# Kernel optimization log

Measured on AMD Instinct MI355X. Metric: run time of the kernel, lower is better.

## Reference

```python
import jax, jax.numpy as jnp
import numpy as np

LN_EPS = 1e-5

def _conv1d_same(x, w, b):
    # x: [B, L, Cin], w: [K, Cin, Cout] (kernel=3, padding=1 -> SAME)
    y = jax.lax.conv_general_dilated(x, w, window_strides=(1,), padding=[(1, 1)],
                                     dimension_numbers=('NWC', 'WIO', 'NWC'))
    return y + b

def _layer_norm(x, g, b):
    mu = jnp.mean(x, axis=-1, keepdims=True)
    var = jnp.var(x, axis=-1, keepdims=True)
    return (x - mu) * jax.lax.rsqrt(var + LN_EPS) * g + b

def _duration_predictor(x, conv1_w, conv1_b, ln1_g, ln1_b, conv2_w, conv2_b, ln2_g, ln2_b, lin_w, lin_b):
    h = jax.nn.relu(_layer_norm(_conv1d_same(x, conv1_w, conv1_b), ln1_g, ln1_b))
    h = jax.nn.relu(_layer_norm(_conv1d_same(h, conv2_w, conv2_b), ln2_g, ln2_b))
    out = jax.nn.relu(h @ lin_w + lin_b)  # [B, L, 1]
    return out[..., 0]  # squeeze -> [B, L]

def _length_regulate(x, dur, T):
    # Equivalent of alignment @ x without materializing [B, T, L] one-hot matrix.
    # Frame t copies phoneme j where cumsum(dur)[j-1] <= t < cumsum(dur)[j].
    ends = jnp.cumsum(dur, axis=-1)          # [B, L]
    total = ends[:, -1]                       # [B]
    t = jnp.arange(T)
    idx = jax.vmap(lambda e: jnp.searchsorted(e, t, side='right'))(ends)  # [B, T]
    idx = jnp.minimum(idx, dur.shape[1] - 1)
    gathered = jnp.take_along_axis(x, idx[:, :, None], axis=1)            # [B, T, D]
    mask = t[None, :] < total[:, None]                                    # [B, T]
    return jnp.where(mask[:, :, None], gathered, 0.0)

def setup_inputs() -> dict:
    key = jax.random.key(0)
    ks = jax.random.split(key, 8)
    B, L, D, F = 64, 512, 256, 256
    inp = {
        'x': jax.random.normal(ks[0], (B, L, D), dtype=jnp.float32),
        'target': jax.random.randint(ks[1], (B, L), 0, 8, dtype=jnp.int32),
        'mel_max_length': 4096,
        'conv1_w': jax.random.normal(ks[2], (3, D, F), dtype=jnp.float32) * 0.05,
        'conv1_b': jnp.zeros((F,), jnp.float32),
        'ln1_g': jnp.ones((F,), jnp.float32),
        'ln1_b': jnp.zeros((F,), jnp.float32),
        'conv2_w': jax.random.normal(ks[3], (3, F, F), dtype=jnp.float32) * 0.05,
        'conv2_b': jnp.zeros((F,), jnp.float32),
        'ln2_g': jnp.ones((F,), jnp.float32),
        'ln2_b': jnp.zeros((F,), jnp.float32),
        'lin_w': jax.random.normal(ks[4], (F, 1), dtype=jnp.float32) * 0.05,
        'lin_b': jnp.zeros((1,), jnp.float32),
    }
    return inp

def reference(x, target, mel_max_length, conv1_w, conv1_b, ln1_g, ln1_b, conv2_w, conv2_b, ln2_g, ln2_b, lin_w, lin_b):
    # Training path of LengthRegulator.forward (target given, dropout eval-mode identity)
    dp_out = _duration_predictor(x, conv1_w, conv1_b, ln1_g, ln1_b, conv2_w, conv2_b, ln2_g, ln2_b, lin_w, lin_b)
    output = _length_regulate(x, target, mel_max_length)  # padded to mel_max_length
    return output, dp_out
```

## Files before the change

### kernel.cpp

```cpp
#include <hip/hip_runtime.h>

#define B 64
#define L 512
#define D 256
#define T 4096
#define LN_EPS 1e-5f

typedef __attribute__((ext_vector_type(8))) short bf16x8;
typedef __attribute__((ext_vector_type(4))) float f32x4;

__device__ __forceinline__ unsigned short f2bf(float f) {
    unsigned int u = __float_as_uint(f);
    unsigned int r = (u + 0x7FFFu + ((u >> 16) & 1u)) >> 16;
    return (unsigned short)r;
}

__global__ __launch_bounds__(256) void prep_kernel(const float* __restrict__ w1,
                                                   const float* __restrict__ w2,
                                                   unsigned short* __restrict__ o1,
                                                   unsigned short* __restrict__ o2,
                                                   const int* __restrict__ target,
                                                   int* __restrict__ ends) {
    const int bid = blockIdx.x;
    const int tid = threadIdx.x;

    if (tid < 64) {
        const int lane = tid;
        const int* trow = target + bid * L;
        int* erow = ends + bid * L;
        int vals[8];
        int base = lane * 8;
#pragma unroll
        for (int j = 0; j < 8; ++j) vals[j] = trow[base + j];
#pragma unroll
        for (int j = 1; j < 8; ++j) vals[j] += vals[j - 1];
        int lsum = vals[7];
        int s = lsum;
#pragma unroll
        for (int off = 1; off < 64; off <<= 1) {
            int v = __shfl_up(s, off, 64);
            if (lane >= off) s += v;
        }
        int excl = s - lsum;
#pragma unroll
        for (int j = 0; j < 8; ++j) erow[base + j] = excl + vals[j];
    }

    if (bid < 48) {
        const int k = bid % 3;
        const int which = (bid / 3) & 1;
        const int d0 = (bid / 6) * 32;
        const float* in = which ? w2 : w1;
        unsigned short* out = which ? o2 : o1;
        const int f = tid;
        for (int dc = 0; dc < 32; dc += 8) {
            unsigned short v[8];
#pragma unroll
            for (int i = 0; i < 8; ++i) v[i] = f2bf(in[(k * 256 + d0 + dc + i) * 256 + f]);
            *(bf16x8*)(out + (k * 256 + f) * 256 + d0 + dc) = *(bf16x8*)v;
        }
    }
}

__global__ __launch_bounds__(256, 2) void dp_fused_kernel(
    const float* __restrict__ x,
    const unsigned short* __restrict__ wT1,
    const unsigned short* __restrict__ wT2,
    const float* __restrict__ c1b, const float* __restrict__ g1, const float* __restrict__ b1,
    const float* __restrict__ c2b, const float* __restrict__ g2, const float* __restrict__ b2,
    const float* __restrict__ lw, const float* __restrict__ lb,
    float* __restrict__ dp)
{
    constexpr int LS = 264;
    __shared__ __align__(16) unsigned short xs[82 * LS];
    __shared__ float ps[80][4], pq[80][4];
    __shared__ float muA[80], rsA[80];

    const int tid = threadIdx.x;
    const int lane = tid & 63;
    const int wid = tid >> 6;
    const int l15 = lane & 15;
    const int g4 = lane >> 4;
    const int b = blockIdx.y;
    const int l0 = blockIdx.x * 64;
    const int col0 = wid * 64;

    for (int i = tid; i < 82 * 32; i += 256) {
        int r = i >> 5, c = i & 31;
        int row = l0 - 9 + r;
        bf16x8 v = {0, 0, 0, 0, 0, 0, 0, 0};
        if (row >= 0 && row < L) {
            const float* xr = x + ((size_t)(b * L + row)) * D + c * 8;
            f32x4 f0 = *(const f32x4*)xr;
            f32x4 f1 = *(const f32x4*)(xr + 4);
            unsigned short t[8] = {f2bf(f0.x), f2bf(f0.y), f2bf(f0.z), f2bf(f0.w),
                                   f2bf(f1.x), f2bf(f1.y), f2bf(f1.z), f2bf(f1.w)};
            v = *(bf16x8*)t;
        }
        *(bf16x8*)(xs + r * LS + c * 8) = v;
    }
    __syncthreads();

    float gv[4], bv[4], biasv[4];
#pragma unroll
    for (int n = 0; n < 4; ++n) {
        int col = col0 + n * 16 + l15;
        biasv[n] = c1b[col];
        gv[n] = g1[col];
        bv[n] = b1[col];
    }

    {
        f32x4 acc[5][4];
#pragma unroll
        for (int m = 0; m < 5; ++m)
#pragma unroll
            for (int n = 0; n < 4; ++n) acc[m][n] = (f32x4){0.f, 0.f, 0.f, 0.f};

        const unsigned short* wbase = wT1 + (col0 + l15) * 256 + g4 * 8;
        bf16x8 bcur[4];
#pragma unroll
        for (int n = 0; n < 4; ++n) bcur[n] = *(const bf16x8*)(wbase + n * 4096);

#pragma unroll 4
        for (int ks = 0; ks < 23; ++ks) {
            const int tap = ks >> 3, kk = ks & 7;
            const int ksn = ks + 1;
            const unsigned short* wp = wbase + (ksn >> 3) * 65536 + (ksn & 7) * 32;
            bf16x8 bnext[4];
#pragma unroll
            for (int n = 0; n < 4; ++n) bnext[n] = *(const bf16x8*)(wp + n * 4096);
            bf16x8 a[5];
#pragma unroll
            for (int m = 0; m < 5; ++m)
                a[m] = *(const bf16x8*)(xs + (m * 16 + l15 + tap) * LS + kk * 32 + g4 * 8);
#pragma unroll
            for (int m = 0; m < 5; ++m)
#pragma unroll
                for (int n = 0; n < 4; ++n)
                    acc[m][n] = __builtin_amdgcn_mfma_f32_16x16x32_bf16(a[m], bcur[n], acc[m][n], 0, 0, 0);
#pragma unroll
            for (int n = 0; n < 4; ++n) bcur[n] = bnext[n];
        }
        {
            bf16x8 a[5];
#pragma unroll
            for (int m = 0; m < 5; ++m)
                a[m] = *(const bf16x8*)(xs + (m * 16 + l15 + 2) * LS + 7 * 32 + g4 * 8);
#pragma unroll
            for (int m = 0; m < 5; ++m)
#pragma unroll
                for (int n = 0; n < 4; ++n)
                    acc[m][n] = __builtin_amdgcn_mfma_f32_16x16x32_bf16(a[m], bcur[n], acc[m][n], 0, 0, 0);
        }

#pragma unroll
        for (int m = 0; m < 5; ++m)
#pragma unroll
            for (int j = 0; j < 4; ++j) {
                float s = 0.f, q = 0.f;
#pragma unroll
                for (int n = 0; n < 4; ++n) {
                    float v = acc[m][n][j] + biasv[n];
                    s += v;
                    q += v * v;
                }
#pragma unroll
                for (int off = 1; off < 16; off <<= 1) {
                    s += __shfl_xor(s, off, 64);
                    q += __shfl_xor(q, off, 64);
                }
                if (l15 == 0) {
                    int row = m * 16 + g4 * 4 + j;
                    ps[row][wid] = s;
                    pq[row][wid] = q;
                }
            }
        __syncthreads();
        if (tid < 80) {
            float s = ps[tid][0] + ps[tid][1] + ps[tid][2] + ps[tid][3];
            float q = pq[tid][0] + pq[tid][1] + pq[tid][2] + pq[tid][3];
            float mu = s * (1.f / 256.f);
            float var = q * (1.f / 256.f) - mu * mu;
            muA[tid] = mu;
            rsA[tid] = rsqrtf(var + LN_EPS);
        }
        __syncthreads();

#pragma unroll
        for (int m = 0; m < 5; ++m)
#pragma unroll
            for (int j = 0; j < 4; ++j) {
                int srow = m * 16 + g4 * 4 + j;
                int hrow = l0 - 8 + srow;
                float mu = muA[srow], rs = rsA[srow];
                bool live = (hrow >= 0) && (hrow < L);
#pragma unroll
                for (int n = 0; n < 4; ++n) {
                    float v = acc[m][n][j] + biasv[n];
                    float y = fmaxf((v - mu) * rs * gv[n] + bv[n], 0.f);
                    if (!live) y = 0.f;
                    xs[srow * LS + col0 + n * 16 + l15] = f2bf(y);
                }
            }
    }
    __syncthreads();

    {
        float lwv[4];
#pragma unroll
        for (int n = 0; n < 4; ++n) {
            int col = col0 + n * 16 + l15;
            biasv[n] = c2b[col];
            gv[n] = g2[col];
            bv[n] = b2[col];
            lwv[n] = lw[col];
        }

        f32x4 acc[4][4];
#pragma unroll
        for (int m = 0; m < 4; ++m)
#pragma unroll
            for (int n = 0; n < 4; ++n) acc[m][n] = (f32x4){0.f, 0.f, 0.f, 0.f};

        const unsigned short* wbase = wT2 + (col0 + l15) * 256 + g4 * 8;
        bf16x8 bcur[4];
#pragma unroll
        for (int n = 0; n < 4; ++n) bcur[n] = *(const bf16x8*)(wbase + n * 4096);

#pragma unroll 4
        for (int ks = 0; ks < 23; ++ks) {
            const int tap = ks >> 3, kk = ks & 7;
            const int ksn = ks + 1;
            const unsigned short* wp = wbase + (ksn >> 3) * 65536 + (ksn & 7) * 32;
            bf16x8 bnext[4];
#pragma unroll
            for (int n = 0; n < 4; ++n) bnext[n] = *(const bf16x8*)(wp + n * 4096);
            bf16x8 a[4];
#pragma unroll
            for (int m = 0; m < 4; ++m)
                a[m] = *(const bf16x8*)(xs + (m * 16 + l15 + tap + 7) * LS + kk * 32 + g4 * 8);
#pragma unroll
            for (int m = 0; m < 4; ++m)
#pragma unroll
                for (int n = 0; n < 4; ++n)
                    acc[m][n] = __builtin_amdgcn_mfma_f32_16x16x32_bf16(a[m], bcur[n], acc[m][n], 0, 0, 0);
#pragma unroll
            for (int n = 0; n < 4; ++n) bcur[n] = bnext[n];
        }
        {
            bf16x8 a[4];
#pragma unroll
            for (int m = 0; m < 4; ++m)
                a[m] = *(const bf16x8*)(xs + (m * 16 + l15 + 2 + 7) * LS + 7 * 32 + g4 * 8);
#pragma unroll
            for (int m = 0; m < 4; ++m)
#pragma unroll
                for (int n = 0; n < 4; ++n)
                    acc[m][n] = __builtin_amdgcn_mfma_f32_16x16x32_bf16(a[m], bcur[n], acc[m][n], 0, 0, 0);
        }

#pragma unroll
        for (int m = 0; m < 4; ++m)
#pragma unroll
            for (int j = 0; j < 4; ++j) {
                float s = 0.f, q = 0.f;
#pragma unroll
                for (int n = 0; n < 4; ++n) {
                    float v = acc[m][n][j] + biasv[n];
                    s += v;
                    q += v * v;
                }
#pragma unroll
                for (int off = 1; off < 16; off <<= 1) {
                    s += __shfl_xor(s, off, 64);
                    q += __shfl_xor(q, off, 64);
                }
                if (l15 == 0) {
                    int row = m * 16 + g4 * 4 + j;
                    ps[row][wid] = s;
                    pq[row][wid] = q;
                }
            }
        __syncthreads();
        if (tid < 64) {
            float s = ps[tid][0] + ps[tid][1] + ps[tid][2] + ps[tid][3];
            float q = pq[tid][0] + pq[tid][1] + pq[tid][2] + pq[tid][3];
            float mu = s * (1.f / 256.f);
            float var = q * (1.f / 256.f) - mu * mu;
            muA[tid] = mu;
            rsA[tid] = rsqrtf(var + LN_EPS);
        }
        __syncthreads();

#pragma unroll
        for (int m = 0; m < 4; ++m)
#pragma unroll
            for (int j = 0; j < 4; ++j) {
                int row = m * 16 + g4 * 4 + j;
                float mu = muA[row], rs = rsA[row];
                float p = 0.f;
#pragma unroll
                for (int n = 0; n < 4; ++n) {
                    float v = acc[m][n][j] + biasv[n];
                    float y = fmaxf((v - mu) * rs * gv[n] + bv[n], 0.f);
                    p += y * lwv[n];
                }
#pragma unroll
                for (int off = 1; off < 16; off <<= 1) p += __shfl_xor(p, off, 64);
                if (l15 == 0) ps[row][wid] = p;
            }
        __syncthreads();
        if (tid < 64)
            dp[b * L + l0 + tid] = fmaxf(ps[tid][0] + ps[tid][1] + ps[tid][2] + ps[tid][3] + lb[0], 0.f);
    }
}

__global__ __launch_bounds__(256) void length_regulate_kernel(
    const float* __restrict__ x, const int* __restrict__ ends, float* __restrict__ out) {
    __shared__ int se[512];
    __shared__ int sidx[256];
    const int tid = threadIdx.x;
    const int lane = tid & 63;
    const int wid = tid >> 6;
    const int b = blockIdx.y;
    const int t0 = blockIdx.x * 256;
    const int* e = ends + b * L;
    se[tid] = e[tid];
    se[tid + 256] = e[tid + 256];
    __syncthreads();
    const int total = se[511];
    {
        int t = t0 + tid;
        int lo = 0, hi = L;
        while (lo < hi) {
            int mid = (lo + hi) >> 1;
            if (se[mid] <= t) lo = mid + 1; else hi = mid;
        }
        sidx[tid] = (lo < L - 1) ? lo : (L - 1);
    }
    __syncthreads();
    const f32x4* x4 = (const f32x4*)(x + (size_t)b * L * D);
    f32x4* o4 = (f32x4*)(out + (size_t)b * T * D);
    const f32x4 z = (f32x4){0.f, 0.f, 0.f, 0.f};
#pragma unroll 4
    for (int rr = 0; rr < 64; ++rr) {
        int row = wid * 64 + rr;
        int t = t0 + row;
        f32x4 v = z;
        if (t < total) v = x4[sidx[row] * 64 + lane];
        o4[(size_t)t * 64 + lane] = v;
    }
}

extern "C" void kernel_launch(void* const* d_in, const int* in_sizes, int n_in,
                              void* d_out, int out_size, void* d_ws, size_t ws_size,
                              hipStream_t stream) {
    const float* x   = (const float*)d_in[0];
    const int* target = (const int*)d_in[1];
    const float* c1w = (const float*)d_in[3];
    const float* c1b = (const float*)d_in[4];
    const float* g1  = (const float*)d_in[5];
    const float* b1  = (const float*)d_in[6];
    const float* c2w = (const float*)d_in[7];
    const float* c2b = (const float*)d_in[8];
    const float* g2  = (const float*)d_in[9];
    const float* b2  = (const float*)d_in[10];
    const float* lw  = (const float*)d_in[11];
    const float* lb  = (const float*)d_in[12];

    float* out = (float*)d_out;
    float* dp  = out + (size_t)B * T * D;

    char* base = (char*)d_out;
    unsigned short* wT1 = (unsigned short*)(base + (32u << 20));
    unsigned short* wT2 = (unsigned short*)(base + (32u << 20) + 393216);
    int* ends = (int*)d_ws;

    prep_kernel<<<dim3(64), dim3(256), 0, stream>>>(c1w, c2w, wT1, wT2, target, ends);
    dp_fused_kernel<<<dim3(L / 64, B), dim3(256), 0, stream>>>(
        x, wT1, wT2, c1b, g1, b1, c2b, g2, b2, lw, lb, dp);
    length_regulate_kernel<<<dim3(T / 256, B), dim3(256), 0, stream>>>(x, ends, out);
}
```

Measured before the change: 399.4 us.

## Merge duration predictor and length regulation into one concurrent launch

Merges the duration-predictor kernel and the length-regulation kernel into a single launch. The first 512 blocks compute the predictor and the remaining 1024 blocks do the gather copy, so the compute-heavy and bandwidth-heavy work can run on the GPU at the same time and one launch gap disappears. The gather loop now issues eight loads before their stores to keep more memory requests in flight. Transposed weight scratch moves from the output buffer to the workspace, since the copy blocks now run concurrently and would overwrite it. The shared-memory union gives every copy block the predictor's large LDS footprint, which may lower occupancy for the memory-bound copy.

```diff
diff --git a/kernel.cpp b/kernel.cpp
--- a/kernel.cpp
+++ b/kernel.cpp
@@ -62,28 +62,84 @@
     }
 }
 
-__global__ __launch_bounds__(256, 2) void dp_fused_kernel(
+union SMem {
+    struct {
+        unsigned short xs[82 * 264];
+        float ps[80][4], pq[80][4];
+        float muA[80], rsA[80];
+    } dp;
+    struct {
+        int se[512];
+        int sidx[256];
+    } lr;
+};
+
+__global__ __launch_bounds__(256, 2) void mega_kernel(
     const float* __restrict__ x,
     const unsigned short* __restrict__ wT1,
     const unsigned short* __restrict__ wT2,
     const float* __restrict__ c1b, const float* __restrict__ g1, const float* __restrict__ b1,
     const float* __restrict__ c2b, const float* __restrict__ g2, const float* __restrict__ b2,
     const float* __restrict__ lw, const float* __restrict__ lb,
+    const int* __restrict__ ends,
+    float* __restrict__ out,
     float* __restrict__ dp)
 {
+    __shared__ SMem sm;
+    const int tid = threadIdx.x;
+
+    if (blockIdx.x >= 512) {
+        const int idx = blockIdx.x - 512;
+        const int lane = tid & 63;
+        const int wid = tid >> 6;
+        const int b = idx >> 4;
+        const int t0 = (idx & 15) * 256;
+        const int* e = ends + b * L;
+        sm.lr.se[tid] = e[tid];
+        sm.lr.se[tid + 256] = e[tid + 256];
+        __syncthreads();
+        const int total = sm.lr.se[511];
+        {
+            int t = t0 + tid;
+            int lo = 0, hi = L;
+            while (lo < hi) {
+                int mid = (lo + hi) >> 1;
+                if (sm.lr.se[mid] <= t) lo = mid + 1; else hi = mid;
+            }
+            sm.lr.sidx[tid] = (lo < L - 1) ? lo : (L - 1);
+        }
+        __syncthreads();
+        const f32x4* x4 = (const f32x4*)(x + (size_t)b * L * D);
+        f32x4* o4 = (f32x4*)(out + (size_t)b * T * D);
+        const f32x4 z = (f32x4){0.f, 0.f, 0.f, 0.f};
+#pragma unroll
+        for (int rc = 0; rc < 8; ++rc) {
+            f32x4 v[8];
+#pragma unroll
+            for (int u = 0; u < 8; ++u) {
+                int row = wid * 64 + rc * 8 + u;
+                int t = t0 + row;
+                v[u] = (t < total) ? x4[sm.lr.sidx[row] * 64 + lane] : z;
+            }
+#pragma unroll
+            for (int u = 0; u < 8; ++u) {
+                int row = wid * 64 + rc * 8 + u;
+                o4[(size_t)(t0 + row) * 64 + lane] = v[u];
+            }
+        }
+        return;
+    }
+
     constexpr int LS = 264;
-    __shared__ __align__(16) unsigned short xs[82 * LS];
-    __shared__ float ps[80][4], pq[80][4];
-    __shared__ float muA[80], rsA[80];
-
-    const int tid = threadIdx.x;
     const int lane = tid & 63;
     const int wid = tid >> 6;
     const int l15 = lane & 15;
     const int g4 = lane >> 4;
-    const int b = blockIdx.y;
-    const int l0 = blockIdx.x * 64;
+    const int b = blockIdx.x >> 3;
+    const int l0 = (blockIdx.x & 7) * 64;
     const int col0 = wid * 64;
+
+    unsigned short* xs = sm.dp.xs;
 
     for (int i = tid; i < 82 * 32; i += 256) {
         int r = i >> 5, c = i & 31;
@@ -172,18 +228,18 @@
                 }
                 if (l15 == 0) {
                     int row = m * 16 + g4 * 4 + j;
-                    ps[row][wid] = s;
-                    pq[row][wid] = q;
+                    sm.dp.ps[row][wid] = s;
+                    sm.dp.pq[row][wid] = q;
                 }
             }
         __syncthreads();
         if (tid < 80) {
-            float s = ps[tid][0] + ps[tid][1] + ps[tid][2] + ps[tid][3];
-            float q = pq[tid][0] + pq[tid][1] + pq[tid][2] + pq[tid][3];
+            float s = sm.dp.ps[tid][0] + sm.dp.ps[tid][1] + sm.dp.ps[tid][2] + sm.dp.ps[tid][3];
+            float q = sm.dp.pq[tid][0] + sm.dp.pq[tid][1] + sm.dp.pq[tid][2] + sm.dp.pq[tid][3];
             float mu = s * (1.f / 256.f);
             float var = q * (1.f / 256.f) - mu * mu;
-            muA[tid] = mu;
-            rsA[tid] = rsqrtf(var + LN_EPS);
+            sm.dp.muA[tid] = mu;
+            sm.dp.rsA[tid] = rsqrtf(var + LN_EPS);
         }
         __syncthreads();
 
@@ -193,7 +249,7 @@
             for (int j = 0; j < 4; ++j) {
                 int srow = m * 16 + g4 * 4 + j;
                 int hrow = l0 - 8 + srow;
-                float mu = muA[srow], rs = rsA[srow];
+                float mu = sm.dp.muA[srow], rs = sm.dp.rsA[srow];
                 bool live = (hrow >= 0) && (hrow < L);
 #pragma unroll
                 for (int n = 0; n < 4; ++n) {
@@ -278,18 +334,18 @@
                 }
                 if (l15 == 0) {
                     int row = m * 16 + g4 * 4 + j;
-                    ps[row][wid] = s;
-                    pq[row][wid] = q;
+                    sm.dp.ps[row][wid] = s;
+                    sm.dp.pq[row][wid] = q;
                 }
             }
         __syncthreads();
         if (tid < 64) {
-            float s = ps[tid][0] + ps[tid][1] + ps[tid][2] + ps[tid][3];
-            float q = pq[tid][0] + pq[tid][1] + pq[tid][2] + pq[tid][3];
+            float s = sm.dp.ps[tid][0] + sm.dp.ps[tid][1] + sm.dp.ps[tid][2] + sm.dp.ps[tid][3];
+            float q = sm.dp.pq[tid][0] + sm.dp.pq[tid][1] + sm.dp.pq[tid][2] + sm.dp.pq[tid][3];
             float mu = s * (1.f / 256.f);
             float var = q * (1.f / 256.f) - mu * mu;
-            muA[tid] = mu;
-            rsA[tid] = rsqrtf(var + LN_EPS);
+            sm.dp.muA[tid] = mu;
+            sm.dp.rsA[tid] = rsqrtf(var + LN_EPS);
         }
         __syncthreads();
 
@@ -298,7 +354,7 @@
 #pragma unroll
             for (int j = 0; j < 4; ++j) {
                 int row = m * 16 + g4 * 4 + j;
-                float mu = muA[row], rs = rsA[row];
+                float mu = sm.dp.muA[row], rs = sm.dp.rsA[row];
                 float p = 0.f;
 #pragma unroll
                 for (int n = 0; n < 4; ++n) {
@@ -308,48 +364,12 @@
                 }
 #pragma unroll
                 for (int off = 1; off < 16; off <<= 1) p += __shfl_xor(p, off, 64);
-                if (l15 == 0) ps[row][wid] = p;
+                if (l15 == 0) sm.dp.ps[row][wid] = p;
             }
         __syncthreads();
         if (tid < 64)
-            dp[b * L + l0 + tid] = fmaxf(ps[tid][0] + ps[tid][1] + ps[tid][2] + ps[tid][3] + lb[0], 0.f);
-    }
-}
-
-__global__ __launch_bounds__(256) void length_regulate_kernel(
-    const float* __restrict__ x, const int* __restrict__ ends, float* __restrict__ out) {
-    __shared__ int se[512];
-    __shared__ int sidx[256];
-    const int tid = threadIdx.x;
-    const int lane = tid & 63;
-    const int wid = tid >> 6;
-    const int b = blockIdx.y;
-    const int t0 = blockIdx.x * 256;
-    const int* e = ends + b * L;
-    se[tid] = e[tid];
-    se[tid + 256] = e[tid + 256];
-    __syncthreads();
-    const int total = se[511];
-    {
-        int t = t0 + tid;
-        int lo = 0, hi = L;
-        while (lo < hi) {
-            int mid = (lo + hi) >> 1;
-            if (se[mid] <= t) lo = mid + 1; else hi = mid;
-        }
-        sidx[tid] = (lo < L - 1) ? lo : (L - 1);
-    }
-    __syncthreads();
-    const f32x4* x4 = (const f32x4*)(x + (size_t)b * L * D);
-    f32x4* o4 = (f32x4*)(out + (size_t)b * T * D);
-    const f32x4 z = (f32x4){0.f, 0.f, 0.f, 0.f};
-#pragma unroll 4
-    for (int rr = 0; rr < 64; ++rr) {
-        int row = wid * 64 + rr;
-        int t = t0 + row;
-        f32x4 v = z;
-        if (t < total) v = x4[sidx[row] * 64 + lane];
-        o4[(size_t)t * 64 + lane] = v;
+            dp[b * L + l0 + tid] =
+                fmaxf(sm.dp.ps[tid][0] + sm.dp.ps[tid][1] + sm.dp.ps[tid][2] + sm.dp.ps[tid][3] + lb[0], 0.f);
     }
 }
 
@@ -372,13 +392,12 @@
     float* out = (float*)d_out;
     float* dp  = out + (size_t)B * T * D;
 
-    char* base = (char*)d_out;
-    unsigned short* wT1 = (unsigned short*)(base + (32u << 20));
-    unsigned short* wT2 = (unsigned short*)(base + (32u << 20) + 393216);
-    int* ends = (int*)d_ws;
+    char* wsb = (char*)d_ws;
+    int* ends = (int*)wsb;
+    unsigned short* wT1 = (unsigned short*)(wsb + 131072);
+    unsigned short* wT2 = (unsigned short*)(wsb + 131072 + 393216);
 
     prep_kernel<<<dim3(64), dim3(256), 0, stream>>>(c1w, c2w, wT1, wT2, target, ends);
-    dp_fused_kernel<<<dim3(L / 64, B), dim3(256), 0, stream>>>(
-        x, wT1, wT2, c1b, g1, b1, c2b, g2, b2, lw, lb, dp);
-    length_regulate_kernel<<<dim3(T / 256, B), dim3(256), 0, stream>>>(x, ends, out);
+    mega_kernel<<<dim3(512 + 1024), dim3(256), 0, stream>>>(
+        x, wT1, wT2, c1b, g1, b1, c2b, g2, b2, lw, lb, ends, out, dp);
 }
```

Result: faster. 383.7 us (-3.9%).
